# Kernel tuning notes

Hardware: AMD Instinct MI355X
Metric: run time of the kernel (lower is better)

## Reference

```python
import jax, jax.numpy as jnp
import numpy as np

# cfg constants (ProposalLayerSoft.__init__)
GRID_SIZE = jnp.array([8000.0, 8000.0, 2000.0], dtype=jnp.float32)   # MULTI_PERSON.SPACE_SIZE (mm)
CUBE_SIZE = jnp.array([128.0, 128.0, 64.0], dtype=jnp.float32)       # MULTI_PERSON.INITIAL_CUBE_SIZE
GRID_CENTER = jnp.array([0.0, 0.0, 300.0], dtype=jnp.float32)        # MULTI_PERSON.SPACE_CENTER
NUM_CAND = 10                                                         # MULTI_PERSON.MAX_PEOPLE_NUM
THRESHOLD = 0.3                                                       # MULTI_PERSON.THRESHOLD


def setup_inputs() -> dict:
    key = jax.random.key(0)
    # root heatmap cube in [0,1): [B, X, Y, Z]
    root_cubes = jax.random.uniform(key, (32, 128, 128, 64), dtype=jnp.float32)
    return {"root_cubes": root_cubes}


def _nms_topk(x):
    """3x3x3 max-pool peak suppression + top-k (repo's nms()).
    x: [B, X, Y, Z] -> (values [B,K], unravel_index [B,K,3] float)."""
    B, X, Y, Z = x.shape
    pooled = jax.lax.reduce_window(
        x, -jnp.inf, jax.lax.max,
        window_dimensions=(1, 3, 3, 3),
        window_strides=(1, 1, 1, 1),
        padding=[(0, 0), (1, 1), (1, 1), (1, 1)],
    )
    peaks = jnp.where(x == pooled, x, 0.0)           # keep only local maxima
    flat = peaks.reshape(B, X * Y * Z)
    topk_values, topk_index = jax.lax.top_k(flat, NUM_CAND)
    # C-order unravel (matches repo's get_index)
    ix = topk_index // (Y * Z)
    iy = (topk_index % (Y * Z)) // Z
    iz = topk_index % Z
    idx = jnp.stack([ix, iy, iz], axis=-1).astype(jnp.float32)  # [B, K, 3]
    return topk_values, idx


def reference(root_cubes):
    x = jax.lax.stop_gradient(root_cubes)  # original calls .detach()
    topk_values, topk_index = _nms_topk(x)
    # get_real_loc: voxel index -> world coords (mm)
    loc = topk_index / (CUBE_SIZE - 1.0) * GRID_SIZE + GRID_CENTER - GRID_SIZE / 2.0
    conf = (topk_values > THRESHOLD).astype(jnp.float32) - 1.0  # col 3
    grid_centers = jnp.concatenate(
        [loc, conf[..., None], topk_values[..., None]], axis=-1
    )  # [B, K, 5]: (x, y, z, valid_flag, score)
    return grid_centers
```

## Files before the change

### kernel.cpp

```cpp
#include <hip/hip_runtime.h>
#include <stdint.h>


#define TPB 256
#define NK 10
#define TY 10
#define BLOCKS_PER_B (4 * TY)
#define WCAP 512
typedef unsigned long long u64;

__device__ __forceinline__ u64 bfly_max_u64(u64 v) {
#pragma unroll
  for (int off = 1; off < 64; off <<= 1) {
    u64 o = __shfl_xor(v, off, 64);
    v = (o > v) ? o : v;
  }
  return v;
}

__device__ __forceinline__ float dpp_nbr_a(float v) {
  return __int_as_float(__builtin_amdgcn_update_dpp(
      0, __float_as_int(v), 0x101, 0xF, 0xF, true));
}
__device__ __forceinline__ float dpp_nbr_b(float v) {
  return __int_as_float(__builtin_amdgcn_update_dpp(
      0, __float_as_int(v), 0x111, 0xF, 0xF, true));
}

__global__ __launch_bounds__(TPB, 5) void peaks_topk(
    const float* __restrict__ in, u64* __restrict__ part) {
  __shared__ u64 cand[4][WCAP];
  __shared__ u64 wtop[4 * NK];
  const int tid = threadIdx.x;
  const int w = tid >> 6, lane = tid & 63;
  const int yi = lane & 15, zq = lane >> 4;
  const int ty = blockIdx.x, b = blockIdx.z;
  const int seg = blockIdx.y * 2 + (w >> 1);
  const int zh = w & 1;
  const int y0 = ty * 14 - 1;
  const int gy = y0 + yi;
  const int cy = min(127, max(0, gy));
  const int x0 = seg << 4;
  const bool emit_ok = (yi >= 1) && (yi <= 14) && (gy <= 127);
  const int zoff = zh * 32 + (zq << 3);
  const int zlo = max(0, zoff - 1);
  const int zhi = min(63, zoff + 8);
  const bool lo_inf = (zq == 0) && (zh == 0);
  const bool hi_inf = (zq == 3) && (zh == 1);
  const float* __restrict__ py = in + ((size_t)b << 20) + ((size_t)cy << 6);

  int wcnt = 0;
  float pm[8], zmLast[8], vC[8], vN[8], vT[8];
  float lN, hN, lT, hT;

  auto loadv = [&](int x, float* v, float& lo, float& hi) {
    const int cx = min(127, max(0, x));
    const float* p = py + ((size_t)cx << 13);
    float4 a = *(const float4*)(p + zoff);
    float4 bb = *(const float4*)(p + zoff + 4);
    v[0] = a.x;  v[1] = a.y;  v[2] = a.z;  v[3] = a.w;
    v[4] = bb.x; v[5] = bb.y; v[6] = bb.z; v[7] = bb.w;
    lo = p[zlo];
    hi = p[zhi];
  };
  auto zmcalc = [&](const float* v, float lo, float hi, float* zm) {
    float vl = __shfl_up(v[7], 16, 64);
    float vr = __shfl_down(v[0], 16, 64);
    vl = (zq == 0) ? (lo_inf ? -1e30f : lo) : vl;
    vr = (zq == 3) ? (hi_inf ? -1e30f : hi) : vr;
    zm[0] = fmaxf(vl, fmaxf(v[0], v[1]));
#pragma unroll
    for (int j = 1; j < 7; ++j)
      zm[j] = fmaxf(v[j - 1], fmaxf(v[j], v[j + 1]));
    zm[7] = fmaxf(v[6], fmaxf(v[7], vr));
  };

  {
    float t0, t1;
    loadv(x0 - 1, vN, t0, t1);
    zmcalc(vN, t0, t1, pm);
    loadv(x0, vC, t0, t1);
    zmcalc(vC, t0, t1, zmLast);
#pragma unroll
    for (int j = 0; j < 8; ++j) pm[j] = fmaxf(pm[j], zmLast[j]);
    loadv(x0 + 1, vN, lN, hN);
  }

#pragma unroll 1
  for (int t = 0; t < 16; ++t) {
    const int x = x0 + t;
    loadv(x + 2, vT, lT, hT);
    float vl = __shfl_up(vN[7], 16, 64);
    float vr = __shfl_down(vN[0], 16, 64);
    vl = (zq == 0) ? (lo_inf ? -1e30f : lN) : vl;
    vr = (zq == 3) ? (hi_inf ? -1e30f : hN) : vr;
#pragma unroll
    for (int j = 0; j < 8; ++j) {
      float a = (j == 0) ? vl : vN[j - 1];
      float c = (j == 7) ? vr : vN[j + 1];
      float zmn = fmaxf(a, fmaxf(vN[j], c));
      float xm = fmaxf(pm[j], zmn);
      pm[j] = fmaxf(zmLast[j], zmn);
      zmLast[j] = zmn;
      float l = dpp_nbr_a(xm);
      float r = dpp_nbr_b(xm);
      float m27 = fmaxf(xm, fmaxf(l, r));
      float v = vC[j];
      const bool pred = emit_ok && (v >= m27);
      u64 mask = __ballot(pred);
      if (pred) {
        unsigned g = ((unsigned)x << 13) | ((unsigned)gy << 6) |
                     (unsigned)(zoff + j);
        u64 key = ((u64)__float_as_uint(v) << 32) | (u64)(unsigned)(~g);
        int ofs = __builtin_amdgcn_mbcnt_hi(
            (unsigned)(mask >> 32),
            __builtin_amdgcn_mbcnt_lo((unsigned)mask, 0));
        int slot = wcnt + ofs;
        if (slot < WCAP) cand[w][slot] = key;
      }
      wcnt += (int)__popcll(mask);
    }
#pragma unroll
    for (int j = 0; j < 8; ++j) {
      vC[j] = vN[j];
      vN[j] = vT[j];
    }
    lN = lT; hN = hT;
  }

  __builtin_amdgcn_s_waitcnt(0);
  const int count = min(wcnt, WCAP);
  u64 c[WCAP / 64];
#pragma unroll
  for (int i = 0; i < WCAP / 64; ++i) {
    int idx = lane + (i << 6);
    c[i] = (idx < count) ? cand[w][idx] : 0;
  }
  u64 mine = 0;
#pragma unroll 1
  for (int r = 0; r < NK; ++r) {
    u64 best = c[0];
#pragma unroll
    for (int i = 1; i < WCAP / 64; ++i) best = (c[i] > best) ? c[i] : best;
    u64 m = bfly_max_u64(best);
    if (m != 0 && best == m) {
#pragma unroll
      for (int i = 0; i < WCAP / 64; ++i)
        if (c[i] == m) c[i] = 0;
    }
    if (lane == r) mine = m;
  }
  if (lane < NK) wtop[w * NK + lane] = mine;
  __syncthreads();

  if (w == 0) {
    u64 c0 = (lane < 4 * NK) ? wtop[lane] : 0;
    u64 mv = 0;
#pragma unroll 1
    for (int r = 0; r < NK; ++r) {
      u64 m = bfly_max_u64(c0);
      if (m != 0 && c0 == m) c0 = 0;
      if (lane == r) mv = m;
    }
    if (lane < NK) {
      const int bi = blockIdx.y * TY + ty;
      part[((size_t)b * BLOCKS_PER_B + bi) * NK + lane] = mv;
    }
  }
}

__global__ __launch_bounds__(64) void final_select(
    const u64* __restrict__ part, float* __restrict__ out) {
  const int lane = threadIdx.x & 63;
  const int b = blockIdx.x;
  const int NKEY = BLOCKS_PER_B * NK;

  const u64* __restrict__ src = part + (size_t)b * NKEY;
  u64 c[7];
#pragma unroll
  for (int i = 0; i < 7; ++i) {
    int idx = lane + (i << 6);
    c[i] = (idx < NKEY) ? src[idx] : 0;
  }
  u64 mine = 0;
#pragma unroll 1
  for (int r = 0; r < NK; ++r) {
    u64 best = c[0];
#pragma unroll
    for (int i = 1; i < 7; ++i) best = (c[i] > best) ? c[i] : best;
    u64 m = bfly_max_u64(best);
    if (m != 0 && best == m) {
#pragma unroll
      for (int i = 0; i < 7; ++i)
        if (c[i] == m) c[i] = 0;
    }
    if (lane == r) mine = m;
  }
  if (lane < NK) {
    float val = 0.0f;
    unsigned g = 0u;
    if (mine != 0) {
      val = __uint_as_float((unsigned)(mine >> 32));
      g = ~((unsigned)mine);
    }
    float fx = (float)(g >> 13) * (8000.0f / 127.0f) - 4000.0f;
    float fy = (float)((g >> 6) & 127u) * (8000.0f / 127.0f) - 4000.0f;
    float fz = (float)(g & 63u) * (2000.0f / 63.0f) - 700.0f;
    float conf = (val > 0.3f) ? 0.0f : -1.0f;
    float* o = out + ((size_t)b * NK + lane) * 5;
    o[0] = fx; o[1] = fy; o[2] = fz; o[3] = conf; o[4] = val;
  }
}

extern "C" void kernel_launch(void* const* d_in, const int* in_sizes, int n_in,
                              void* d_out, int out_size, void* d_ws, size_t ws_size,
                              hipStream_t stream) {
  const float* in = (const float*)d_in[0];
  float* out = (float*)d_out;
  u64* part = (u64*)d_ws;

  const int B = in_sizes[0] >> 20;
  dim3 gridA(TY, 4, (unsigned)B);
  peaks_topk<<<gridA, dim3(TPB), 0, stream>>>(in, part);
  final_select<<<dim3((unsigned)B), dim3(64), 0, stream>>>(part, out);
}
```

Before: 218.3 us.

## Add threshold-filtered first pass with exact full-scan fallback per batch

The peak search becomes a two-pass scheme. The first pass runs the full 27-neighbour max test only for voxels above a high threshold (0.999), skipping whole waves and columns when nothing qualifies, and atomically counts the candidates it finds per batch. A second, unfiltered pass runs only for batches with fewer than the top-k count, so results stay exact for any input. The sliding-window reuse of z/x partial maxima is replaced by recomputing the full window from three resident planes, trading extra ALU work on the rare hot path for simpler branch skipping. The cost is an extra memset, an extra launch and per-batch atomics, and the input is read twice whenever the fallback triggers.

```diff
diff --git a/kernel.cpp b/kernel.cpp
--- a/kernel.cpp
+++ b/kernel.cpp
@@ -7,6 +7,7 @@
 #define TY 10
 #define BLOCKS_PER_B (4 * TY)
 #define WCAP 512
+#define THRV 0.999f
 typedef unsigned long long u64;
 
 __device__ __forceinline__ u64 bfly_max_u64(u64 v) {
@@ -27,14 +28,21 @@
       0, __float_as_int(v), 0x111, 0xF, 0xF, true));
 }
 
+template <bool PASS1>
 __global__ __launch_bounds__(TPB, 5) void peaks_topk(
-    const float* __restrict__ in, u64* __restrict__ part) {
+    const float* __restrict__ in, u64* __restrict__ part,
+    unsigned* __restrict__ cnt) {
   __shared__ u64 cand[4][WCAP];
   __shared__ u64 wtop[4 * NK];
+  __shared__ unsigned wcnts[4];
+  const int b = blockIdx.z;
+  if (!PASS1) {
+    if (cnt[b] >= NK) return;
+  }
   const int tid = threadIdx.x;
   const int w = tid >> 6, lane = tid & 63;
   const int yi = lane & 15, zq = lane >> 4;
-  const int ty = blockIdx.x, b = blockIdx.z;
+  const int ty = blockIdx.x;
   const int seg = blockIdx.y * 2 + (w >> 1);
   const int zh = w & 1;
   const int y0 = ty * 14 - 1;
@@ -50,8 +58,8 @@
   const float* __restrict__ py = in + ((size_t)b << 20) + ((size_t)cy << 6);
 
   int wcnt = 0;
-  float pm[8], zmLast[8], vC[8], vN[8], vT[8];
-  float lN, hN, lT, hT;
+  float vP[8], vC[8], vN[8];
+  float loP, hiP, loC, hiC, loN, hiN;
 
   auto loadv = [&](int x, float* v, float& lo, float& hi) {
     const int cx = min(127, max(0, x));
@@ -63,69 +71,73 @@
     lo = p[zlo];
     hi = p[zhi];
   };
-  auto zmcalc = [&](const float* v, float lo, float hi, float* zm) {
-    float vl = __shfl_up(v[7], 16, 64);
-    float vr = __shfl_down(v[0], 16, 64);
-    vl = (zq == 0) ? (lo_inf ? -1e30f : lo) : vl;
-    vr = (zq == 3) ? (hi_inf ? -1e30f : hi) : vr;
-    zm[0] = fmaxf(vl, fmaxf(v[0], v[1]));
-#pragma unroll
-    for (int j = 1; j < 7; ++j)
-      zm[j] = fmaxf(v[j - 1], fmaxf(v[j], v[j + 1]));
-    zm[7] = fmaxf(v[6], fmaxf(v[7], vr));
-  };
-
-  {
-    float t0, t1;
-    loadv(x0 - 1, vN, t0, t1);
-    zmcalc(vN, t0, t1, pm);
-    loadv(x0, vC, t0, t1);
-    zmcalc(vC, t0, t1, zmLast);
-#pragma unroll
-    for (int j = 0; j < 8; ++j) pm[j] = fmaxf(pm[j], zmLast[j]);
-    loadv(x0 + 1, vN, lN, hN);
-  }
+
+  loadv(x0 - 1, vP, loP, hiP);
+  loadv(x0,     vC, loC, hiC);
+  loadv(x0 + 1, vN, loN, hiN);
 
 #pragma unroll 1
   for (int t = 0; t < 16; ++t) {
     const int x = x0 + t;
-    loadv(x + 2, vT, lT, hT);
-    float vl = __shfl_up(vN[7], 16, 64);
-    float vr = __shfl_down(vN[0], 16, 64);
-    vl = (zq == 0) ? (lo_inf ? -1e30f : lN) : vl;
-    vr = (zq == 3) ? (hi_inf ? -1e30f : hN) : vr;
+    bool anyc;
+    if (PASS1) {
+      float cm = fmaxf(fmaxf(fmaxf(vC[0], vC[1]), fmaxf(vC[2], vC[3])),
+                       fmaxf(fmaxf(vC[4], vC[5]), fmaxf(vC[6], vC[7])));
+      anyc = emit_ok && (cm > THRV);
+    } else {
+      anyc = emit_ok;
+    }
+    if (__ballot(anyc)) {
+      float vlP = __shfl_up(vP[7], 16, 64), vrP = __shfl_down(vP[0], 16, 64);
+      float vlC = __shfl_up(vC[7], 16, 64), vrC = __shfl_down(vC[0], 16, 64);
+      float vlN = __shfl_up(vN[7], 16, 64), vrN = __shfl_down(vN[0], 16, 64);
+      vlP = (zq == 0) ? (lo_inf ? -1e30f : loP) : vlP;
+      vrP = (zq == 3) ? (hi_inf ? -1e30f : hiP) : vrP;
+      vlC = (zq == 0) ? (lo_inf ? -1e30f : loC) : vlC;
+      vrC = (zq == 3) ? (hi_inf ? -1e30f : hiC) : vrC;
+      vlN = (zq == 0) ? (lo_inf ? -1e30f : loN) : vlN;
+      vrN = (zq == 3) ? (hi_inf ? -1e30f : hiN) : vrN;
+#pragma unroll
+      for (int j = 0; j < 8; ++j) {
+        const float v = vC[j];
+        const bool pj = emit_ok && (PASS1 ? (v > THRV) : true);
+        if (__ballot(pj)) {
+          float aP = (j == 0) ? vlP : vP[j - 1];
+          float cP = (j == 7) ? vrP : vP[j + 1];
+          float aC = (j == 0) ? vlC : vC[j - 1];
+          float cC = (j == 7) ? vrC : vC[j + 1];
+          float aN = (j == 0) ? vlN : vN[j - 1];
+          float cN = (j == 7) ? vrN : vN[j + 1];
+          float zP = fmaxf(aP, fmaxf(vP[j], cP));
+          float zC = fmaxf(aC, fmaxf(v, cC));
+          float zN = fmaxf(aN, fmaxf(vN[j], cN));
+          float xm = fmaxf(zP, fmaxf(zC, zN));
+          float l = dpp_nbr_a(xm);
+          float r = dpp_nbr_b(xm);
+          float m27 = fmaxf(xm, fmaxf(l, r));
+          const bool pred = pj && (v >= m27);
+          u64 mask = __ballot(pred);
+          if (pred) {
+            unsigned g = ((unsigned)x << 13) | ((unsigned)gy << 6) |
+                         (unsigned)(zoff + j);
+            u64 key = ((u64)__float_as_uint(v) << 32) | (u64)(unsigned)(~g);
+            int ofs = __builtin_amdgcn_mbcnt_hi(
+                (unsigned)(mask >> 32),
+                __builtin_amdgcn_mbcnt_lo((unsigned)mask, 0));
+            int slot = wcnt + ofs;
+            if (slot < WCAP) cand[w][slot] = key;
+          }
+          wcnt += (int)__popcll(mask);
+        }
+      }
+    }
 #pragma unroll
     for (int j = 0; j < 8; ++j) {
-      float a = (j == 0) ? vl : vN[j - 1];
-      float c = (j == 7) ? vr : vN[j + 1];
-      float zmn = fmaxf(a, fmaxf(vN[j], c));
-      float xm = fmaxf(pm[j], zmn);
-      pm[j] = fmaxf(zmLast[j], zmn);
-      zmLast[j] = zmn;
-      float l = dpp_nbr_a(xm);
-      float r = dpp_nbr_b(xm);
-      float m27 = fmaxf(xm, fmaxf(l, r));
-      float v = vC[j];
-      const bool pred = emit_ok && (v >= m27);
-      u64 mask = __ballot(pred);
-      if (pred) {
-        unsigned g = ((unsigned)x << 13) | ((unsigned)gy << 6) |
-                     (unsigned)(zoff + j);
-        u64 key = ((u64)__float_as_uint(v) << 32) | (u64)(unsigned)(~g);
-        int ofs = __builtin_amdgcn_mbcnt_hi(
-            (unsigned)(mask >> 32),
-            __builtin_amdgcn_mbcnt_lo((unsigned)mask, 0));
-        int slot = wcnt + ofs;
-        if (slot < WCAP) cand[w][slot] = key;
-      }
-      wcnt += (int)__popcll(mask);
-    }
-#pragma unroll
-    for (int j = 0; j < 8; ++j) {
+      vP[j] = vC[j];
       vC[j] = vN[j];
-      vN[j] = vT[j];
-    }
-    lN = lT; hN = hT;
+    }
+    loP = loC; hiP = hiC; loC = loN; hiC = hiN;
+    loadv(x + 2, vN, loN, hiN);
   }
 
   __builtin_amdgcn_s_waitcnt(0);
@@ -151,6 +163,7 @@
     if (lane == r) mine = m;
   }
   if (lane < NK) wtop[w * NK + lane] = mine;
+  if (lane == 0) wcnts[w] = (unsigned)wcnt;
   __syncthreads();
 
   if (w == 0) {
@@ -165,6 +178,10 @@
     if (lane < NK) {
       const int bi = blockIdx.y * TY + ty;
       part[((size_t)b * BLOCKS_PER_B + bi) * NK + lane] = mv;
+    }
+    if (PASS1 && lane == 0) {
+      unsigned s = wcnts[0] + wcnts[1] + wcnts[2] + wcnts[3];
+      if (s) atomicAdd(&cnt[b], s);
     }
   }
 }
@@ -218,9 +235,13 @@
   const float* in = (const float*)d_in[0];
   float* out = (float*)d_out;
   u64* part = (u64*)d_ws;
-
   const int B = in_sizes[0] >> 20;
+  unsigned* cnt =
+      (unsigned*)((char*)d_ws + (size_t)B * BLOCKS_PER_B * NK * sizeof(u64));
+
+  hipMemsetAsync(cnt, 0, (size_t)B * sizeof(unsigned), stream);
   dim3 gridA(TY, 4, (unsigned)B);
-  peaks_topk<<<gridA, dim3(TPB), 0, stream>>>(in, part);
+  peaks_topk<true><<<gridA, dim3(TPB), 0, stream>>>(in, part, cnt);
+  peaks_topk<false><<<gridA, dim3(TPB), 0, stream>>>(in, part, cnt);
   final_select<<<dim3((unsigned)B), dim3(64), 0, stream>>>(part, out);
 }
```

Result: slower. 223.7 us (+2.5%).
